# Optimization experiments

Measured on AMD Instinct MI355X. Metric: run time of the kernel, lower is better.

## Reference

```python
import jax, jax.numpy as jnp
import numpy as np

B, Q, KV = 8, 16, 2048
NQ, NK, NV, H = 512, 512, 512, 512

def setup_inputs() -> dict:
    key = jax.random.key(0)
    k = jax.random.split(key, 7)
    s = 0.02
    return {
        "query": jax.random.normal(k[0], (B, Q, NQ), jnp.float32),
        "keys": jax.random.normal(k[1], (B, KV, NK), jnp.float32),
        "values": jax.random.normal(k[2], (B, KV, NV), jnp.float32),
        "W_weight": jax.random.normal(k[3], (H, NQ + NK), jnp.float32) * s,
        "W_bias": jax.random.normal(k[4], (H,), jnp.float32) * s,
        "v_weight": jax.random.normal(k[5], (1, H), jnp.float32) * s,
        "v_bias": jax.random.normal(k[6], (1,), jnp.float32) * s,
    }

def reference(query, keys, values, W_weight, W_bias, v_weight, v_bias):
    # Split W over the concat axis: cat([query, keys]) @ W^T == query@Wq^T + keys@Wk^T
    Wq = W_weight[:, :NQ]   # [H, Nq]
    Wk = W_weight[:, NQ:]   # [H, Nk]
    q_part = jnp.einsum('bqn,hn->bqh', query, Wq)   # [B,Q,H]
    k_part = jnp.einsum('bkn,hn->bkh', keys, Wk)    # [B,KV,H]
    # broadcast-add -> [B,KV,Q,H], tanh, project to scalar energy
    energy = jnp.tanh(k_part[:, :, None, :] + q_part[:, None, :, :] + W_bias)
    e = jnp.einsum('bkqh,h->bkq', energy, v_weight[0]) + v_bias[0]  # [B,KV,Q]
    scores = jax.nn.softmax(e, axis=1)              # softmax over KV
    # output = (values^T @ scores)^T -> [B,Q,Nv]
    output = jnp.einsum('bkn,bkq->bqn', values, scores)
    return output
```

## Files before the change

### kernel.cpp

```cpp
#include <hip/hip_runtime.h>
#include <cstddef>

using bf16x8  = __attribute__((ext_vector_type(8))) short;
using f32x4   = __attribute__((ext_vector_type(4))) float;
using ushort8 = __attribute__((ext_vector_type(8))) unsigned short;

#define GLL16(gp, lp) __builtin_amdgcn_global_load_lds( \
    (const __attribute__((address_space(1))) unsigned int*)(const void*)(gp), \
    (__attribute__((address_space(3))) unsigned int*)(void*)(lp), 16, 0, 0)

__device__ __forceinline__ float exp2_f(float x){ float r; asm("v_exp_f32 %0, %1" : "=v"(r) : "v"(x)); return r; }
__device__ __forceinline__ float rcp_f (float x){ float r; asm("v_rcp_f32 %0, %1" : "=v"(r) : "v"(x)); return r; }

__device__ __forceinline__ unsigned short f2bf(float f){
  unsigned int u = __float_as_uint(f);
  u = u + 0x7FFFu + ((u >> 16) & 1u);
  return (unsigned short)(u >> 16);
}

#define KEYS_N   8388608
#define QUERY_N  65536
#define SCALE_2LOG2E 2.885390081777927f

#define OFF_EPART     0u
#define OFF_KEYS_BF   0u
#define OFF_QUERY_BF  16777216u
#define OFF_WK_BF     16908288u
#define OFF_WQ_BF     17432576u
#define OFF_EKB       17956864u
#define OFF_EQB       51511296u
#define OFF_SC        51773440u
#define OFF_PART      52822016u

__global__ __launch_bounds__(256) void k_convert(
    const float* __restrict__ query, const float* __restrict__ keys,
    const float* __restrict__ W,
    unsigned short* __restrict__ keys_bf, unsigned short* __restrict__ query_bf,
    unsigned short* __restrict__ wk_bf, unsigned short* __restrict__ wq_bf)
{
  int idx = (blockIdx.x * 256 + threadIdx.x) * 8;
  const float* src;
  unsigned short* dst;
  if (idx < KEYS_N) { src = keys + idx; dst = keys_bf + idx; }
  else if (idx < KEYS_N + QUERY_N) { int e = idx - KEYS_N; src = query + e; dst = query_bf + e; }
  else {
    int e = idx - (KEYS_N + QUERY_N);
    int h = e >> 10, c = e & 1023;
    src = W + e;
    dst = (c < 512) ? (wq_bf + h * 512 + c) : (wk_bf + h * 512 + (c - 512));
  }
  float4 a = *(const float4*)src;
  float4 b = *(const float4*)(src + 4);
  ushort8 o;
  o[0]=f2bf(a.x); o[1]=f2bf(a.y); o[2]=f2bf(a.z); o[3]=f2bf(a.w);
  o[4]=f2bf(b.x); o[5]=f2bf(b.y); o[6]=f2bf(b.z); o[7]=f2bf(b.w);
  *(ushort8*)dst = o;
}

__global__ __launch_bounds__(256) void k_gemm(
    const unsigned short* __restrict__ keys_bf, const unsigned short* __restrict__ query_bf,
    const unsigned short* __restrict__ wk_bf, const unsigned short* __restrict__ wq_bf,
    const float* __restrict__ w_bias,
    float* __restrict__ ekb, float* __restrict__ eqb)
{
  __shared__ short As[2][128 * 64];
  __shared__ short Bs[2][128 * 64];

  const int tid = threadIdx.x;
  const int l = tid & 63;
  const int w = tid >> 6;
  const int by = blockIdx.y;
  const bool isq = (by == 128);
  const int n0 = blockIdx.x * 128;

  const unsigned short* Aptr = isq ? query_bf : (keys_bf + (size_t)by * 128 * 512);
  const unsigned short* Bptr = (isq ? wq_bf : wk_bf) + (size_t)n0 * 512;

  const int eo_base = w * 2048 + l * 8;

  f32x4 acc[4][4];
  #pragma unroll
  for (int i = 0; i < 4; ++i)
    #pragma unroll
    for (int j = 0; j < 4; ++j)
      acc[i][j] = (f32x4){0.f, 0.f, 0.f, 0.f};

  auto stage = [&](int buf, int kt) {
    const int k0 = kt * 64;
    #pragma unroll
    for (int r = 0; r < 4; ++r) {
      const int eo = eo_base + r * 512;
      const int row = eo >> 6;
      const int col = eo & 63;
      GLL16(Aptr + row * 512 + k0 + col, &As[buf][w * 2048 + r * 512]);
      GLL16(Bptr + row * 512 + k0 + col, &Bs[buf][w * 2048 + r * 512]);
    }
  };

  const int wm = w >> 1, wn = w & 1;
  const int fr = l & 15;
  const int fg = l >> 4;

  auto compute = [&](int buf) {
    #pragma unroll
    for (int ks = 0; ks < 2; ++ks) {
      bf16x8 af[4], bfv[4];
      #pragma unroll
      for (int i = 0; i < 4; ++i) {
        const int ar = wm * 64 + i * 16 + fr;
        af[i]  = *(const bf16x8*)&As[buf][ar * 64 + ks * 32 + fg * 8];
        const int br = wn * 64 + i * 16 + fr;
        bfv[i] = *(const bf16x8*)&Bs[buf][br * 64 + ks * 32 + fg * 8];
      }
      #pragma unroll
      for (int i = 0; i < 4; ++i)
        #pragma unroll
        for (int j = 0; j < 4; ++j)
          acc[i][j] = __builtin_amdgcn_mfma_f32_16x16x32_bf16(af[i], bfv[j], acc[i][j], 0, 0, 0);
    }
  };

  stage(0, 0);
  for (int kt = 0; kt < 8; ++kt) {
    __syncthreads();
    if (kt < 7) stage((kt + 1) & 1, kt + 1);
    compute(kt & 1);
  }

  #pragma unroll
  for (int j = 0; j < 4; ++j) {
    const int gh = n0 + wn * 64 + j * 16 + fr;
    const float bias = isq ? 0.f : w_bias[gh];
    #pragma unroll
    for (int i = 0; i < 4; ++i) {
      #pragma unroll
      for (int r = 0; r < 4; ++r) {
        const int gm = wm * 64 + i * 16 + fg * 4 + r;
        const float ev = exp2_f((acc[i][j][r] + bias) * SCALE_2LOG2E);
        if (isq) eqb[gm * 512 + gh] = ev;
        else     ekb[((size_t)by * 128 + gm) * 512 + gh] = ev;
      }
    }
  }
}

__global__ __launch_bounds__(256) void k_energy(
    const float* __restrict__ ekb, const float* __restrict__ eqb,
    const float* __restrict__ vw, float* __restrict__ e_part)
{
  __shared__ float eqs[16 * 128];
  const int tid = threadIdx.x;
  const int bid = blockIdx.x;
  const int hc = bid & 3;
  const int ktg = (bid >> 2) & 31;
  const int b = bid >> 7;
  const int h0 = hc * 128;

  {
    const int q = tid >> 4, c0 = (tid & 15) * 8;
    const float* src = eqb + (size_t)(b * 16 + q) * 512 + h0 + c0;
    *(float4*)&eqs[q * 128 + c0]     = *(const float4*)src;
    *(float4*)&eqs[q * 128 + c0 + 4] = *(const float4*)(src + 4);
  }

  const int w = tid >> 6, l = tid & 63;
  const int kt = ktg * 4 + w;
  const int g = l & 3, kl = l >> 2;
  const int k = kt * 16 + kl;

  float ek[32], vv[32];
  const float* ekrow = ekb + ((size_t)(b * 2048 + k)) * 512 + h0;
  #pragma unroll
  for (int s = 0; s < 4; ++s) {
    *(float4*)&ek[s * 8]     = *(const float4*)(ekrow + s * 32 + g * 4);
    *(float4*)&ek[s * 8 + 4] = *(const float4*)(ekrow + s * 32 + 16 + g * 4);
    *(float4*)&vv[s * 8]     = *(const float4*)(vw + h0 + s * 32 + g * 4);
    *(float4*)&vv[s * 8 + 4] = *(const float4*)(vw + h0 + s * 32 + 16 + g * 4);
  }
  __syncthreads();

  const size_t epbase = (size_t)hc * 262144 + ((size_t)(b * 2048 + k)) * 16;

  #pragma unroll 2
  for (int q = 0; q < 16; ++q) {
    float a0 = 0.f, a1 = 0.f;
    #pragma unroll
    for (int s = 0; s < 4; ++s) {
      const float* er = &eqs[q * 128 + s * 32 + g * 4];
      const float4 E0 = *(const float4*)er;
      const float4 E1 = *(const float4*)(er + 16);
      a0 = fmaf(vv[s*8+0], rcp_f(fmaf(ek[s*8+0], E0.x, 1.f)), a0);
      a1 = fmaf(vv[s*8+1], rcp_f(fmaf(ek[s*8+1], E0.y, 1.f)), a1);
      a0 = fmaf(vv[s*8+2], rcp_f(fmaf(ek[s*8+2], E0.z, 1.f)), a0);
      a1 = fmaf(vv[s*8+3], rcp_f(fmaf(ek[s*8+3], E0.w, 1.f)), a1);
      a0 = fmaf(vv[s*8+4], rcp_f(fmaf(ek[s*8+4], E1.x, 1.f)), a0);
      a1 = fmaf(vv[s*8+5], rcp_f(fmaf(ek[s*8+5], E1.y, 1.f)), a1);
      a0 = fmaf(vv[s*8+6], rcp_f(fmaf(ek[s*8+6], E1.z, 1.f)), a0);
      a1 = fmaf(vv[s*8+7], rcp_f(fmaf(ek[s*8+7], E1.w, 1.f)), a1);
    }
    float a = a0 + a1;
    a += __shfl_xor(a, 1, 64);
    a += __shfl_xor(a, 2, 64);
    if (g == 0) e_part[epbase + q] = -2.f * a;
  }
}

__global__ __launch_bounds__(256) void k_softmax(
    const float* __restrict__ e_part, float* __restrict__ sc)
{
  const int b = blockIdx.x >> 4, q = blockIdx.x & 15;
  const int base = b * 32768 + q;
  const int tid = threadIdx.x;
  __shared__ float redm[4], reds[4];

  float vals[8];
  float mx = -1e30f;
  #pragma unroll
  for (int i = 0; i < 8; ++i) {
    const int x = base + (tid + i * 256) * 16;
    vals[i] = (e_part[x] + e_part[x + 262144]) + (e_part[x + 524288] + e_part[x + 786432]);
    mx = fmaxf(mx, vals[i]);
  }
  #pragma unroll
  for (int msk = 1; msk < 64; msk <<= 1) mx = fmaxf(mx, __shfl_xor(mx, msk, 64));
  if ((tid & 63) == 0) redm[tid >> 6] = mx;
  __syncthreads();
  mx = fmaxf(fmaxf(redm[0], redm[1]), fmaxf(redm[2], redm[3]));

  float ex[8], sum = 0.f;
  #pragma unroll
  for (int i = 0; i < 8; ++i) { ex[i] = __expf(vals[i] - mx); sum += ex[i]; }
  #pragma unroll
  for (int msk = 1; msk < 64; msk <<= 1) sum += __shfl_xor(sum, msk, 64);
  if ((tid & 63) == 0) reds[tid >> 6] = sum;
  __syncthreads();
  sum = reds[0] + reds[1] + reds[2] + reds[3];
  const float r = 1.f / sum;
  #pragma unroll
  for (int i = 0; i < 8; ++i) sc[base + (tid + i * 256) * 16] = ex[i] * r;
}

__global__ __launch_bounds__(128) void k_pv(
    const float* __restrict__ values, const float* __restrict__ sc,
    float* __restrict__ part)
{
  __shared__ float s_sc[64 * 16];
  const int c = blockIdx.x, b = blockIdx.y;
  const int tid = threadIdx.x;
  const float* ssrc = sc + (b * 2048 + c * 64) * 16;
  #pragma unroll
  for (int i = 0; i < 2; ++i)
    *(float4*)&s_sc[tid * 4 + i * 512] = *(const float4*)&ssrc[tid * 4 + i * 512];
  __syncthreads();

  float4 acc[16];
  #pragma unroll
  for (int q = 0; q < 16; ++q) acc[q] = make_float4(0.f, 0.f, 0.f, 0.f);

  const float* vbase = values + ((size_t)(b * 2048 + c * 64)) * 512 + tid * 4;
  #pragma unroll 2
  for (int kk = 0; kk < 64; ++kk) {
    const float4 v4 = *(const float4*)(vbase + (size_t)kk * 512);
    #pragma unroll
    for (int g = 0; g < 4; ++g) {
      const float4 s4 = *(const float4*)&s_sc[kk * 16 + g * 4];
      #define PV_ACC(qi, sv) { float4& a = acc[qi]; a.x += v4.x*(sv); a.y += v4.y*(sv); a.z += v4.z*(sv); a.w += v4.w*(sv); }
      PV_ACC(g*4+0, s4.x); PV_ACC(g*4+1, s4.y); PV_ACC(g*4+2, s4.z); PV_ACC(g*4+3, s4.w);
      #undef PV_ACC
    }
  }
  float* pbase = part + ((size_t)((b * 32 + c) * 16)) * 512 + tid * 4;
  #pragma unroll
  for (int q = 0; q < 16; ++q) *(float4*)(pbase + q * 512) = acc[q];
}

__global__ __launch_bounds__(256) void k_reduce(
    const float* __restrict__ part, float* __restrict__ out)
{
  const int o = blockIdx.x * 256 + threadIdx.x;
  const int n = o & 511;
  const int bq = o >> 9;
  const int q = bq & 15;
  const int b = bq >> 4;
  const float* p = part + ((size_t)(b * 32 * 16 + q)) * 512 + n;
  float s = 0.f;
  #pragma unroll
  for (int c2 = 0; c2 < 32; ++c2) s += p[(size_t)c2 * 16 * 512];
  out[o] = s;
}

extern "C" void kernel_launch(void* const* d_in, const int* in_sizes, int n_in,
                              void* d_out, int out_size, void* d_ws, size_t ws_size,
                              hipStream_t stream)
{
  const float* query  = (const float*)d_in[0];
  const float* keys   = (const float*)d_in[1];
  const float* values = (const float*)d_in[2];
  const float* W      = (const float*)d_in[3];
  const float* w_bias = (const float*)d_in[4];
  const float* vw     = (const float*)d_in[5];

  char* ws = (char*)d_ws;
  unsigned short* keys_bf  = (unsigned short*)(ws + OFF_KEYS_BF);
  unsigned short* query_bf = (unsigned short*)(ws + OFF_QUERY_BF);
  unsigned short* wk_bf    = (unsigned short*)(ws + OFF_WK_BF);
  unsigned short* wq_bf    = (unsigned short*)(ws + OFF_WQ_BF);
  float* ekb    = (float*)(ws + OFF_EKB);
  float* eqb    = (float*)(ws + OFF_EQB);
  float* e_part = (float*)(ws + OFF_EPART);
  float* sc     = (float*)(ws + OFF_SC);
  float* part   = (float*)(ws + OFF_PART);

  hipLaunchKernelGGL(k_convert, dim3(4384), dim3(256), 0, stream,
                     query, keys, W, keys_bf, query_bf, wk_bf, wq_bf);
  hipLaunchKernelGGL(k_gemm, dim3(4, 129), dim3(256), 0, stream,
                     keys_bf, query_bf, wk_bf, wq_bf, w_bias, ekb, eqb);
  hipLaunchKernelGGL(k_energy, dim3(1024), dim3(256), 0, stream, ekb, eqb, vw, e_part);
  hipLaunchKernelGGL(k_softmax, dim3(128), dim3(256), 0, stream, e_part, sc);
  hipLaunchKernelGGL(k_pv, dim3(32, 8), dim3(128), 0, stream, values, sc, part);
  hipLaunchKernelGGL(k_reduce, dim3(256), dim3(256), 0, stream, part, (float*)d_out);
}
```

Before: 96.62 us.

## Fuse keys GEMM with energy computation via LDS and split PV over more threads

The keys projection GEMM is fused with the tanh-energy reduction. The exp'd key projection tile stays in LDS, in a union with the GEMM staging buffers, instead of making a 32MB round trip through global memory. The query GEMM becomes its own small kernel. The -2 scale is folded into the v weights. The PV kernel now uses 256 threads that split the KV chunk in two, doubling the partials the reduce kernel sums, to raise parallelism. The risk is the larger LDS footprint and longer-running blocks in the fused kernel, and more partial traffic in the reduce.

```diff
diff --git a/kernel.cpp b/kernel.cpp
--- a/kernel.cpp
+++ b/kernel.cpp
@@ -22,15 +22,14 @@
 #define QUERY_N  65536
 #define SCALE_2LOG2E 2.885390081777927f
 
-#define OFF_EPART     0u
 #define OFF_KEYS_BF   0u
 #define OFF_QUERY_BF  16777216u
 #define OFF_WK_BF     16908288u
 #define OFF_WQ_BF     17432576u
-#define OFF_EKB       17956864u
-#define OFF_EQB       51511296u
-#define OFF_SC        51773440u
-#define OFF_PART      52822016u
+#define OFF_EQB       17956864u
+#define OFF_EPART     18219008u
+#define OFF_SC        22413312u
+#define OFF_PART      23461888u
 
 __global__ __launch_bounds__(256) void k_convert(
     const float* __restrict__ query, const float* __restrict__ keys,
@@ -57,60 +56,44 @@
   *(ushort8*)dst = o;
 }
 
-__global__ __launch_bounds__(256) void k_gemm(
-    const unsigned short* __restrict__ keys_bf, const unsigned short* __restrict__ query_bf,
-    const unsigned short* __restrict__ wk_bf, const unsigned short* __restrict__ wq_bf,
-    const float* __restrict__ w_bias,
-    float* __restrict__ ekb, float* __restrict__ eqb)
-{
-  __shared__ short As[2][128 * 64];
-  __shared__ short Bs[2][128 * 64];
-
+__global__ __launch_bounds__(256) void k_qgemm(
+    const unsigned short* __restrict__ query_bf, const unsigned short* __restrict__ wq_bf,
+    float* __restrict__ eqb)
+{
+  __shared__ short As[2][8192];
+  __shared__ short Bs[2][8192];
   const int tid = threadIdx.x;
-  const int l = tid & 63;
-  const int w = tid >> 6;
-  const int by = blockIdx.y;
-  const bool isq = (by == 128);
+  const int l = tid & 63, w = tid >> 6;
   const int n0 = blockIdx.x * 128;
-
-  const unsigned short* Aptr = isq ? query_bf : (keys_bf + (size_t)by * 128 * 512);
-  const unsigned short* Bptr = (isq ? wq_bf : wk_bf) + (size_t)n0 * 512;
-
+  const unsigned short* Bptr = wq_bf + (size_t)n0 * 512;
   const int eo_base = w * 2048 + l * 8;
 
   f32x4 acc[4][4];
   #pragma unroll
   for (int i = 0; i < 4; ++i)
     #pragma unroll
-    for (int j = 0; j < 4; ++j)
-      acc[i][j] = (f32x4){0.f, 0.f, 0.f, 0.f};
+    for (int j = 0; j < 4; ++j) acc[i][j] = (f32x4){0.f,0.f,0.f,0.f};
 
   auto stage = [&](int buf, int kt) {
     const int k0 = kt * 64;
     #pragma unroll
     for (int r = 0; r < 4; ++r) {
       const int eo = eo_base + r * 512;
-      const int row = eo >> 6;
-      const int col = eo & 63;
-      GLL16(Aptr + row * 512 + k0 + col, &As[buf][w * 2048 + r * 512]);
+      const int row = eo >> 6, col = eo & 63;
+      GLL16(query_bf + row * 512 + k0 + col, &As[buf][w * 2048 + r * 512]);
       GLL16(Bptr + row * 512 + k0 + col, &Bs[buf][w * 2048 + r * 512]);
     }
   };
-
   const int wm = w >> 1, wn = w & 1;
-  const int fr = l & 15;
-  const int fg = l >> 4;
-
+  const int fr = l & 15, fg = l >> 4;
   auto compute = [&](int buf) {
     #pragma unroll
     for (int ks = 0; ks < 2; ++ks) {
       bf16x8 af[4], bfv[4];
       #pragma unroll
       for (int i = 0; i < 4; ++i) {
-        const int ar = wm * 64 + i * 16 + fr;
-        af[i]  = *(const bf16x8*)&As[buf][ar * 64 + ks * 32 + fg * 8];
-        const int br = wn * 64 + i * 16 + fr;
-        bfv[i] = *(const bf16x8*)&Bs[buf][br * 64 + ks * 32 + fg * 8];
+        af[i]  = *(const bf16x8*)&As[buf][(wm*64 + i*16 + fr) * 64 + ks*32 + fg*8];
+        bfv[i] = *(const bf16x8*)&Bs[buf][(wn*64 + i*16 + fr) * 64 + ks*32 + fg*8];
       }
       #pragma unroll
       for (int i = 0; i < 4; ++i)
@@ -119,89 +102,153 @@
           acc[i][j] = __builtin_amdgcn_mfma_f32_16x16x32_bf16(af[i], bfv[j], acc[i][j], 0, 0, 0);
     }
   };
-
   stage(0, 0);
   for (int kt = 0; kt < 8; ++kt) {
     __syncthreads();
     if (kt < 7) stage((kt + 1) & 1, kt + 1);
     compute(kt & 1);
   }
-
   #pragma unroll
   for (int j = 0; j < 4; ++j) {
-    const int gh = n0 + wn * 64 + j * 16 + fr;
-    const float bias = isq ? 0.f : w_bias[gh];
-    #pragma unroll
-    for (int i = 0; i < 4; ++i) {
+    const int gh = n0 + wn*64 + j*16 + fr;
+    #pragma unroll
+    for (int i = 0; i < 4; ++i)
       #pragma unroll
       for (int r = 0; r < 4; ++r) {
-        const int gm = wm * 64 + i * 16 + fg * 4 + r;
-        const float ev = exp2_f((acc[i][j][r] + bias) * SCALE_2LOG2E);
-        if (isq) eqb[gm * 512 + gh] = ev;
-        else     ekb[((size_t)by * 128 + gm) * 512 + gh] = ev;
-      }
-    }
-  }
-}
-
-__global__ __launch_bounds__(256) void k_energy(
-    const float* __restrict__ ekb, const float* __restrict__ eqb,
+        const int gm = wm*64 + i*16 + fg*4 + r;
+        eqb[gm * 512 + gh] = exp2_f(acc[i][j][r] * SCALE_2LOG2E);
+      }
+  }
+}
+
+struct FusedSM {
+  union {
+    struct { short A[2][8192]; short B[2][8192]; } g;
+    float ek[128 * 132];
+  } u;
+  float eqs[16 * 128];
+};
+
+__global__ __launch_bounds__(256, 2) void k_fused(
+    const unsigned short* __restrict__ keys_bf, const unsigned short* __restrict__ wk_bf,
+    const float* __restrict__ w_bias, const float* __restrict__ eqb,
     const float* __restrict__ vw, float* __restrict__ e_part)
 {
-  __shared__ float eqs[16 * 128];
+  __shared__ FusedSM sm;
   const int tid = threadIdx.x;
-  const int bid = blockIdx.x;
-  const int hc = bid & 3;
-  const int ktg = (bid >> 2) & 31;
-  const int b = bid >> 7;
+  const int l = tid & 63, w = tid >> 6;
+  const int hc = blockIdx.x;
+  const int by = blockIdx.y;
   const int h0 = hc * 128;
-
+  const int b  = by >> 4;
+
+  const unsigned short* Aptr = keys_bf + (size_t)by * 128 * 512;
+  const unsigned short* Bptr = wk_bf + (size_t)h0 * 512;
+  const int eo_base = w * 2048 + l * 8;
+
+  f32x4 acc[4][4];
+  #pragma unroll
+  for (int i = 0; i < 4; ++i)
+    #pragma unroll
+    for (int j = 0; j < 4; ++j) acc[i][j] = (f32x4){0.f,0.f,0.f,0.f};
+
+  auto stage = [&](int buf, int kt) {
+    const int k0 = kt * 64;
+    #pragma unroll
+    for (int r = 0; r < 4; ++r) {
+      const int eo = eo_base + r * 512;
+      const int row = eo >> 6, col = eo & 63;
+      GLL16(Aptr + row * 512 + k0 + col, &sm.u.g.A[buf][w * 2048 + r * 512]);
+      GLL16(Bptr + row * 512 + k0 + col, &sm.u.g.B[buf][w * 2048 + r * 512]);
+    }
+  };
+  const int wm = w >> 1, wn = w & 1;
+  const int fr = l & 15, fg = l >> 4;
+  auto compute = [&](int buf) {
+    #pragma unroll
+    for (int ks = 0; ks < 2; ++ks) {
+      bf16x8 af[4], bfv[4];
+      #pragma unroll
+      for (int i = 0; i < 4; ++i) {
+        af[i]  = *(const bf16x8*)&sm.u.g.A[buf][(wm*64 + i*16 + fr) * 64 + ks*32 + fg*8];
+        bfv[i] = *(const bf16x8*)&sm.u.g.B[buf][(wn*64 + i*16 + fr) * 64 + ks*32 + fg*8];
+      }
+      #pragma unroll
+      for (int i = 0; i < 4; ++i)
+        #pragma unroll
+        for (int j = 0; j < 4; ++j)
+          acc[i][j] = __builtin_amdgcn_mfma_f32_16x16x32_bf16(af[i], bfv[j], acc[i][j], 0, 0, 0);
+    }
+  };
+  stage(0, 0);
+  for (int kt = 0; kt < 8; ++kt) {
+    __syncthreads();
+    if (kt < 7) stage((kt + 1) & 1, kt + 1);
+    compute(kt & 1);
+  }
+  __syncthreads();
+
+  #pragma unroll
+  for (int j = 0; j < 4; ++j) {
+    const int lc = wn*64 + j*16 + fr;
+    const float bias = w_bias[h0 + lc];
+    #pragma unroll
+    for (int i = 0; i < 4; ++i)
+      #pragma unroll
+      for (int r = 0; r < 4; ++r) {
+        const int lm = wm*64 + i*16 + fg*4 + r;
+        sm.u.ek[lm * 132 + lc] = exp2_f((acc[i][j][r] + bias) * SCALE_2LOG2E);
+      }
+  }
   {
     const int q = tid >> 4, c0 = (tid & 15) * 8;
     const float* src = eqb + (size_t)(b * 16 + q) * 512 + h0 + c0;
-    *(float4*)&eqs[q * 128 + c0]     = *(const float4*)src;
-    *(float4*)&eqs[q * 128 + c0 + 4] = *(const float4*)(src + 4);
-  }
-
-  const int w = tid >> 6, l = tid & 63;
-  const int kt = ktg * 4 + w;
+    *(float4*)&sm.eqs[q * 128 + c0]     = *(const float4*)src;
+    *(float4*)&sm.eqs[q * 128 + c0 + 4] = *(const float4*)(src + 4);
+  }
   const int g = l & 3, kl = l >> 2;
-  const int k = kt * 16 + kl;
-
-  float ek[32], vv[32];
-  const float* ekrow = ekb + ((size_t)(b * 2048 + k)) * 512 + h0;
+  float vv[32];
   #pragma unroll
   for (int s = 0; s < 4; ++s) {
-    *(float4*)&ek[s * 8]     = *(const float4*)(ekrow + s * 32 + g * 4);
-    *(float4*)&ek[s * 8 + 4] = *(const float4*)(ekrow + s * 32 + 16 + g * 4);
-    *(float4*)&vv[s * 8]     = *(const float4*)(vw + h0 + s * 32 + g * 4);
-    *(float4*)&vv[s * 8 + 4] = *(const float4*)(vw + h0 + s * 32 + 16 + g * 4);
-  }
-  __syncthreads();
-
-  const size_t epbase = (size_t)hc * 262144 + ((size_t)(b * 2048 + k)) * 16;
-
-  #pragma unroll 2
-  for (int q = 0; q < 16; ++q) {
-    float a0 = 0.f, a1 = 0.f;
+    const float4 a0 = *(const float4*)(vw + h0 + s*32 + g*4);
+    const float4 a1 = *(const float4*)(vw + h0 + s*32 + 16 + g*4);
+    vv[s*8+0]=-2.f*a0.x; vv[s*8+1]=-2.f*a0.y; vv[s*8+2]=-2.f*a0.z; vv[s*8+3]=-2.f*a0.w;
+    vv[s*8+4]=-2.f*a1.x; vv[s*8+5]=-2.f*a1.y; vv[s*8+6]=-2.f*a1.z; vv[s*8+7]=-2.f*a1.w;
+  }
+  __syncthreads();
+
+  #pragma unroll
+  for (int p = 0; p < 2; ++p) {
+    const int lr = w * 32 + p * 16 + kl;
+    float ek[32];
     #pragma unroll
     for (int s = 0; s < 4; ++s) {
-      const float* er = &eqs[q * 128 + s * 32 + g * 4];
-      const float4 E0 = *(const float4*)er;
-      const float4 E1 = *(const float4*)(er + 16);
-      a0 = fmaf(vv[s*8+0], rcp_f(fmaf(ek[s*8+0], E0.x, 1.f)), a0);
-      a1 = fmaf(vv[s*8+1], rcp_f(fmaf(ek[s*8+1], E0.y, 1.f)), a1);
-      a0 = fmaf(vv[s*8+2], rcp_f(fmaf(ek[s*8+2], E0.z, 1.f)), a0);
-      a1 = fmaf(vv[s*8+3], rcp_f(fmaf(ek[s*8+3], E0.w, 1.f)), a1);
-      a0 = fmaf(vv[s*8+4], rcp_f(fmaf(ek[s*8+4], E1.x, 1.f)), a0);
-      a1 = fmaf(vv[s*8+5], rcp_f(fmaf(ek[s*8+5], E1.y, 1.f)), a1);
-      a0 = fmaf(vv[s*8+6], rcp_f(fmaf(ek[s*8+6], E1.z, 1.f)), a0);
-      a1 = fmaf(vv[s*8+7], rcp_f(fmaf(ek[s*8+7], E1.w, 1.f)), a1);
-    }
-    float a = a0 + a1;
-    a += __shfl_xor(a, 1, 64);
-    a += __shfl_xor(a, 2, 64);
-    if (g == 0) e_part[epbase + q] = -2.f * a;
+      *(float4*)&ek[s*8]     = *(const float4*)&sm.u.ek[lr*132 + s*32 + g*4];
+      *(float4*)&ek[s*8 + 4] = *(const float4*)&sm.u.ek[lr*132 + s*32 + 16 + g*4];
+    }
+    const size_t epbase = (size_t)hc * 262144 + ((size_t)(by * 128 + lr)) * 16;
+    #pragma unroll 2
+    for (int q = 0; q < 16; ++q) {
+      float a0 = 0.f, a1 = 0.f;
+      #pragma unroll
+      for (int s = 0; s < 4; ++s) {
+        const float* er = &sm.eqs[q * 128 + s * 32 + g * 4];
+        const float4 E0 = *(const float4*)er;
+        const float4 E1 = *(const float4*)(er + 16);
+        a0 = fmaf(vv[s*8+0], rcp_f(fmaf(ek[s*8+0], E0.x, 1.f)), a0);
+        a1 = fmaf(vv[s*8+1], rcp_f(fmaf(ek[s*8+1], E0.y, 1.f)), a1);
+        a0 = fmaf(vv[s*8+2], rcp_f(fmaf(ek[s*8+2], E0.z, 1.f)), a0);
+        a1 = fmaf(vv[s*8+3], rcp_f(fmaf(ek[s*8+3], E0.w, 1.f)), a1);
+        a0 = fmaf(vv[s*8+4], rcp_f(fmaf(ek[s*8+4], E1.x, 1.f)), a0);
+        a1 = fmaf(vv[s*8+5], rcp_f(fmaf(ek[s*8+5], E1.y, 1.f)), a1);
+        a0 = fmaf(vv[s*8+6], rcp_f(fmaf(ek[s*8+6], E1.z, 1.f)), a0);
+        a1 = fmaf(vv[s*8+7], rcp_f(fmaf(ek[s*8+7], E1.w, 1.f)), a1);
+      }
+      float a = a0 + a1;
+      a += __shfl_xor(a, 1, 64);
+      a += __shfl_xor(a, 2, 64);
+      if (g == 0) e_part[epbase + q] = a;
+    }
   }
 }
 
@@ -240,7 +287,7 @@
   for (int i = 0; i < 8; ++i) sc[base + (tid + i * 256) * 16] = ex[i] * r;
 }
 
-__global__ __launch_bounds__(128) void k_pv(
+__global__ __launch_bounds__(256) void k_pv(
     const float* __restrict__ values, const float* __restrict__ sc,
     float* __restrict__ part)
 {
@@ -248,28 +295,29 @@
   const int c = blockIdx.x, b = blockIdx.y;
   const int tid = threadIdx.x;
   const float* ssrc = sc + (b * 2048 + c * 64) * 16;
-  #pragma unroll
-  for (int i = 0; i < 2; ++i)
-    *(float4*)&s_sc[tid * 4 + i * 512] = *(const float4*)&ssrc[tid * 4 + i * 512];
-  __syncthreads();
-
+  *(float4*)&s_sc[tid * 4] = *(const float4*)&ssrc[tid * 4];
+  __syncthreads();
+
+  const int kg = tid >> 7, nt = tid & 127;
   float4 acc[16];
   #pragma unroll
   for (int q = 0; q < 16; ++q) acc[q] = make_float4(0.f, 0.f, 0.f, 0.f);
 
-  const float* vbase = values + ((size_t)(b * 2048 + c * 64)) * 512 + tid * 4;
+  const float* vbase = values + ((size_t)(b * 2048 + c * 64 + kg * 32)) * 512 + nt * 4;
   #pragma unroll 2
-  for (int kk = 0; kk < 64; ++kk) {
+  for (int kk = 0; kk < 32; ++kk) {
     const float4 v4 = *(const float4*)(vbase + (size_t)kk * 512);
+    const int ks = (kg * 32 + kk) * 16;
     #pragma unroll
     for (int g = 0; g < 4; ++g) {
-      const float4 s4 = *(const float4*)&s_sc[kk * 16 + g * 4];
+      const float4 s4 = *(const float4*)&s_sc[ks + g * 4];
       #define PV_ACC(qi, sv) { float4& a = acc[qi]; a.x += v4.x*(sv); a.y += v4.y*(sv); a.z += v4.z*(sv); a.w += v4.w*(sv); }
       PV_ACC(g*4+0, s4.x); PV_ACC(g*4+1, s4.y); PV_ACC(g*4+2, s4.z); PV_ACC(g*4+3, s4.w);
       #undef PV_ACC
     }
   }
-  float* pbase = part + ((size_t)((b * 32 + c) * 16)) * 512 + tid * 4;
+  const int cc = c * 2 + kg;
+  float* pbase = part + ((size_t)((b * 64 + cc) * 16)) * 512 + nt * 4;
   #pragma unroll
   for (int q = 0; q < 16; ++q) *(float4*)(pbase + q * 512) = acc[q];
 }
@@ -279,13 +327,12 @@
 {
   const int o = blockIdx.x * 256 + threadIdx.x;
   const int n = o & 511;
-  const int bq = o >> 9;
-  const int q = bq & 15;
-  const int b = bq >> 4;
-  const float* p = part + ((size_t)(b * 32 * 16 + q)) * 512 + n;
+  const int q = (o >> 9) & 15;
+  const int b = o >> 13;
+  const float* p = part + ((size_t)(b * 64 * 16 + q)) * 512 + n;
   float s = 0.f;
   #pragma unroll
-  for (int c2 = 0; c2 < 32; ++c2) s += p[(size_t)c2 * 16 * 512];
+  for (int cc = 0; cc < 64; ++cc) s += p[(size_t)cc * 16 * 512];
   out[o] = s;
 }
 
@@ -305,7 +352,6 @@
   unsigned short* query_bf = (unsigned short*)(ws + OFF_QUERY_BF);
   unsigned short* wk_bf    = (unsigned short*)(ws + OFF_WK_BF);
   unsigned short* wq_bf    = (unsigned short*)(ws + OFF_WQ_BF);
-  float* ekb    = (float*)(ws + OFF_EKB);
   float* eqb    = (float*)(ws + OFF_EQB);
   float* e_part = (float*)(ws + OFF_EPART);
   float* sc     = (float*)(ws + OFF_SC);
@@ -313,10 +359,10 @@
 
   hipLaunchKernelGGL(k_convert, dim3(4384), dim3(256), 0, stream,
                      query, keys, W, keys_bf, query_bf, wk_bf, wq_bf);
-  hipLaunchKernelGGL(k_gemm, dim3(4, 129), dim3(256), 0, stream,
-                     keys_bf, query_bf, wk_bf, wq_bf, w_bias, ekb, eqb);
-  hipLaunchKernelGGL(k_energy, dim3(1024), dim3(256), 0, stream, ekb, eqb, vw, e_part);
+  hipLaunchKernelGGL(k_qgemm, dim3(4), dim3(256), 0, stream, query_bf, wq_bf, eqb);
+  hipLaunchKernelGGL(k_fused, dim3(4, 128), dim3(256), 0, stream,
+                     keys_bf, wk_bf, w_bias, eqb, vw, e_part);
   hipLaunchKernelGGL(k_softmax, dim3(128), dim3(256), 0, stream, e_part, sc);
-  hipLaunchKernelGGL(k_pv, dim3(32, 8), dim3(128), 0, stream, values, sc, part);
+  hipLaunchKernelGGL(k_pv, dim3(32, 8), dim3(256), 0, stream, values, sc, part);
   hipLaunchKernelGGL(k_reduce, dim3(256), dim3(256), 0, stream, part, (float*)d_out);
 }
```

Result: slower. 148.1 us (+53.3%).
